# Kernel tuning notes

Hardware: AMD Instinct MI355X
Metric: run time of the kernel (lower is better)

Reference implementation:

```python
import jax, jax.numpy as jnp
import numpy as np

B, TAU, M, NX, NY = 256, 128, 3, 8, 8
N = NX + NY                 # 16 total sensors
D = 2 * N * N               # d_model = 512
NHEAD = 8
DFF = 2048


def _layer_norm(x, g, b, eps=1e-5):
    mu = jnp.mean(x, axis=-1, keepdims=True)
    var = jnp.mean((x - mu) ** 2, axis=-1, keepdims=True)
    return (x - mu) / jnp.sqrt(var + eps) * g + b


def _mha(x, wi, bi, wo, bo):
    Bq, S, Dm = x.shape
    hd = Dm // NHEAD
    qkv = x @ wi.T + bi                         # (B,S,3D)
    q, k, v = jnp.split(qkv, 3, axis=-1)
    sh = lambda t: t.reshape(Bq, S, NHEAD, hd).transpose(0, 2, 1, 3)
    q, k, v = sh(q), sh(k), sh(v)
    att = jax.nn.softmax(jnp.einsum('bhqd,bhkd->bhqk', q, k) / jnp.sqrt(jnp.float32(hd)), axis=-1)
    o = jnp.einsum('bhqk,bhkd->bhqd', att, v).transpose(0, 2, 1, 3).reshape(Bq, S, Dm)
    return o @ wo.T + bo


def poly_roots(c):
    # companion-matrix roots; c[..., 0] is the leading coefficient
    n = c.shape[-1] - 1
    first = (-c[..., 1:] / c[..., :1])[..., None, :]                      # (..., 1, n)
    below = jnp.broadcast_to(jnp.eye(n - 1, n, dtype=c.dtype), c.shape[:-1] + (n - 1, n))
    return jnp.linalg.eigvals(jnp.concatenate([first, below], axis=-2))   # (..., n)


def root_music_doa(Rz, m):
    # Rz: (B, n, n) Hermitian PSD (gram + eps*I) -> eigh == eig sorted by |lambda|
    n = Rz.shape[-1]
    w, v = jnp.linalg.eigh(Rz)                  # ascending real eigenvalues
    Un = v[..., : n - m]                        # noise subspace (smallest n-m)
    F = Un @ jnp.conj(jnp.swapaxes(Un, -1, -2))
    # sum of each diagonal, offsets -(n-1)..(n-1) -> 2n-1 poly coefficients
    coeffs = jnp.stack([jnp.sum(jnp.diagonal(F, offset=o, axis1=-2, axis2=-1), axis=-1)
                        for o in range(-(n - 1), n)], axis=-1)
    roots = poly_roots(coeffs)                  # (B, 2n-2)
    # sort by closeness to unit circle; push roots with |r|>=1 to the back
    keyv = jnp.abs(jnp.abs(roots) - 1.0) + jnp.where(jnp.abs(roots) < 1.0, 0.0, 1e6)
    sel = jnp.take_along_axis(roots, jnp.argsort(keyv, axis=-1)[..., :m], axis=-1)
    # dist=0.5, f=1 -> 1/(2*pi*dist*f) = 1/pi
    return jnp.arcsin(jnp.angle(sel) / jnp.pi)  # (B, m)


def setup_inputs() -> dict:
    key = jax.random.key(0)
    ks = jax.random.split(key, 12)
    rn = lambda k, s: 0.02 * jax.random.normal(k, s, jnp.float32)
    return {
        'Rx_tau': jax.random.normal(ks[0], (B, TAU, 2 * N, N), jnp.float32),
        'in_proj_w': rn(ks[1], (3 * D, D)), 'in_proj_b': jnp.zeros((3 * D,), jnp.float32),
        'out_proj_w': rn(ks[2], (D, D)), 'out_proj_b': jnp.zeros((D,), jnp.float32),
        'ln1_g': jnp.ones((D,), jnp.float32), 'ln1_b': jnp.zeros((D,), jnp.float32),
        'ffn_w1': rn(ks[3], (DFF, D)), 'ffn_b1': jnp.zeros((DFF,), jnp.float32),
        'ffn_w2': rn(ks[4], (D, DFF)), 'ffn_b2': jnp.zeros((D,), jnp.float32),
        'ln2_g': jnp.ones((D,), jnp.float32), 'ln2_b': jnp.zeros((D,), jnp.float32),
        'fcx_w': rn(ks[5], (2 * NX * NX, D)), 'fcx_b': jnp.zeros((2 * NX * NX,), jnp.float32),
        'fcy_w': rn(ks[6], (2 * NY * NY, D)), 'fcy_b': jnp.zeros((2 * NY * NY,), jnp.float32),
        'mlp_w1': rn(ks[7], (256, 2 * M)), 'mlp_b1': jnp.zeros((256,), jnp.float32),
        'mlp_w2': rn(ks[8], (256, 256)), 'mlp_b2': jnp.zeros((256,), jnp.float32),
        'mlp_w3': rn(ks[9], (2 * M, 256)), 'mlp_b3': jnp.zeros((2 * M,), jnp.float32),
    }


def reference(Rx_tau, in_proj_w, in_proj_b, out_proj_w, out_proj_b, ln1_g, ln1_b,
              ffn_w1, ffn_b1, ffn_w2, ffn_b2, ln2_g, ln2_b,
              fcx_w, fcx_b, fcy_w, fcy_b,
              mlp_w1, mlp_b1, mlp_w2, mlp_b2, mlp_w3, mlp_b3):
    x = Rx_tau.reshape(Rx_tau.shape[0], -1, D)  # (B, tau, 512)
    # post-LN TransformerEncoderLayer (eval: dropout off)
    x = _layer_norm(x + _mha(x, in_proj_w, in_proj_b, out_proj_w, out_proj_b), ln1_g, ln1_b)
    ff = jnp.maximum(x @ ffn_w1.T + ffn_b1, 0.0) @ ffn_w2.T + ffn_b2
    x = _layer_norm(x + ff, ln2_g, ln2_b)
    x = jnp.mean(x, axis=1)                     # (B, D)
    Rx = (x @ fcx_w.T + fcx_b).reshape(-1, 2 * NX, NX)
    Ry = (x @ fcy_w.T + fcy_b).reshape(-1, 2 * NY, NY)
    Kx = jax.lax.complex(Rx[:, :NX], Rx[:, NX:])
    Ky = jax.lax.complex(Ry[:, :NY], Ry[:, NY:])
    # gram_diagonal_overload: K^H K + eps*I, eps=1
    Rz_x = jnp.einsum('bji,bjk->bik', jnp.conj(Kx), Kx) + jnp.eye(NX, dtype=Kx.dtype)
    Rz_y = jnp.einsum('bji,bjk->bik', jnp.conj(Ky), Ky) + jnp.eye(NY, dtype=Ky.dtype)
    doa_t = root_music_doa(Rz_x, M)
    doa_p = root_music_doa(Rz_y, M)
    h = jnp.concatenate([doa_t, doa_p], axis=-1).astype(jnp.float32)  # (B, 2M)
    h = jnp.maximum(h @ mlp_w1.T + mlp_b1, 0.0)
    h = jnp.maximum(h @ mlp_w2.T + mlp_b2, 0.0)
    outs = h @ mlp_w3.T + mlp_b3
    return outs[:, :M], outs[:, M:]
```

## Files before the change

kernel.cpp:

```cpp
#include <hip/hip_runtime.h>
#include <math.h>

#define S_LEN 128
#define D_MODEL 512
#define B_SZ 256
#define NHEADS 8
#define HD 64
#define DFFN 2048
#define PI_D 3.14159265358979323846
#define DK_ITERS 128
#define JACOBI_SWEEPS 9

typedef _Float16 f16x8 __attribute__((ext_vector_type(8)));
typedef _Float16 f16x4 __attribute__((ext_vector_type(4)));
typedef float f32x4 __attribute__((ext_vector_type(4)));

__device__ __forceinline__ void gl_lds(const _Float16* g, _Float16* l) {
    __builtin_amdgcn_global_load_lds(
        (const __attribute__((address_space(1))) void*)g,
        (__attribute__((address_space(3))) void*)l, 16, 0, 0);
}

__global__ __launch_bounds__(256) void cvt_split(const float* __restrict__ in,
        _Float16* __restrict__ hi, _Float16* __restrict__ lo, int n4)
{
    const int i = blockIdx.x * 256 + threadIdx.x;
    if (i >= n4) return;
    float4 v = ((const float4*)in)[i];
    f16x4 h, l;
    _Float16 h0 = (_Float16)v.x; h[0] = h0; l[0] = (_Float16)(v.x - (float)h0);
    _Float16 h1 = (_Float16)v.y; h[1] = h1; l[1] = (_Float16)(v.y - (float)h1);
    _Float16 h2 = (_Float16)v.z; h[2] = h2; l[2] = (_Float16)(v.z - (float)h2);
    _Float16 h3 = (_Float16)v.w; h[3] = h3; l[3] = (_Float16)(v.w - (float)h3);
    ((f16x4*)hi)[i] = h;
    ((f16x4*)lo)[i] = l;
}

template<int OUTMODE>
__global__ __launch_bounds__(256) void gemm_mfma(
        const _Float16* __restrict__ Ahg, const _Float16* __restrict__ Alg,
        const _Float16* __restrict__ Whg, const _Float16* __restrict__ Wlg,
        const float* __restrict__ bias, float* __restrict__ Cf,
        _Float16* __restrict__ Ch, _Float16* __restrict__ Cl,
        int M, int N, int K)
{
    __shared__ _Float16 lds[2][4][4096];
    const int t = threadIdx.x;
    const int lane = t & 63;
    const int w = t >> 6;
    const int wr = w >> 1, wc = w & 1;
    const int row0 = blockIdx.y * 128, col0 = blockIdx.x * 128;

    const _Float16* gptr[4] = { Ahg, Alg, Whg, Wlg };
    const int rbase = (w < 2) ? row0 : col0;
    const _Float16* gsrc = gptr[w];
    const int lr = lane >> 2;
    const int lc = (lane & 3) * 8;

    auto stage = [&](int buf, int kt) {
        const _Float16* srcb = gsrc + (size_t)(rbase + lr) * K + (kt << 5) + lc;
        _Float16* dstb = &lds[buf][w][lane * 8];
#pragma unroll
        for (int p = 0; p < 8; ++p)
            gl_lds(srcb + (size_t)p * 16 * K, dstb + p * 512);
    };

    f32x4 acc[4][4];
#pragma unroll
    for (int m = 0; m < 4; ++m)
#pragma unroll
        for (int n = 0; n < 4; ++n) acc[m][n] = (f32x4)0.f;

    const int NT = K >> 5;
    stage(0, 0);
    float bv[4];
#pragma unroll
    for (int n = 0; n < 4; ++n) bv[n] = bias[col0 + wc * 64 + n * 16 + (lane & 15)];

    __syncthreads();

    const int kf = (lane >> 4) * 8;
    for (int kt = 0; kt < NT; ++kt) {
        const int cur = kt & 1;
        if (kt + 1 < NT) stage(cur ^ 1, kt + 1);
        f16x8 afh[4], afl[4], bfh[4], bfl[4];
#pragma unroll
        for (int m = 0; m < 4; ++m) {
            const int e = (wr * 64 + m * 16 + (lane & 15)) * 32 + kf;
            afh[m] = *(const f16x8*)&lds[cur][0][e];
            afl[m] = *(const f16x8*)&lds[cur][1][e];
        }
#pragma unroll
        for (int n = 0; n < 4; ++n) {
            const int e = (wc * 64 + n * 16 + (lane & 15)) * 32 + kf;
            bfh[n] = *(const f16x8*)&lds[cur][2][e];
            bfl[n] = *(const f16x8*)&lds[cur][3][e];
        }
#pragma unroll
        for (int m = 0; m < 4; ++m)
#pragma unroll
            for (int n = 0; n < 4; ++n) {
                acc[m][n] = __builtin_amdgcn_mfma_f32_16x16x32_f16(afh[m], bfh[n], acc[m][n], 0, 0, 0);
                acc[m][n] = __builtin_amdgcn_mfma_f32_16x16x32_f16(afh[m], bfl[n], acc[m][n], 0, 0, 0);
                acc[m][n] = __builtin_amdgcn_mfma_f32_16x16x32_f16(afl[m], bfh[n], acc[m][n], 0, 0, 0);
            }
        __syncthreads();
    }

#pragma unroll
    for (int m = 0; m < 4; ++m) {
        const int rowc = row0 + wr * 64 + m * 16 + ((lane >> 4) << 2);
#pragma unroll
        for (int n = 0; n < 4; ++n) {
            const int colc = col0 + wc * 64 + n * 16 + (lane & 15);
#pragma unroll
            for (int j = 0; j < 4; ++j) {
                float v = acc[m][n][j] + bv[n];
                if (OUTMODE == 2) {
                    v = fmaxf(v, 0.f);
                    const size_t idx = (size_t)(rowc + j) * N + colc;
                    _Float16 h = (_Float16)v;
                    Ch[idx] = h;
                    Cl[idx] = (_Float16)(v - (float)h);
                } else {
                    Cf[(size_t)(rowc + j) * N + colc] = v;
                }
            }
        }
    }
}

template<int RELU>
__global__ __launch_bounds__(256) void gemm_bias(const float* __restrict__ A,
        const float* __restrict__ W, const float* __restrict__ bias,
        float* __restrict__ C, int M, int N, int K)
{
    __shared__ float As[8][128];
    __shared__ float Ws[8][128];
    const int tid = threadIdx.x;
    const int tn = tid & 15, tm = tid >> 4;
    const int row0 = blockIdx.y * 128, col0 = blockIdx.x * 128;
    const int lrr = tid >> 1, lcc = (tid & 1) * 4;
    const float* Ap = A + (size_t)(row0 + lrr) * K + lcc;
    const float* Wp = W + (size_t)(col0 + lrr) * K + lcc;
    float acc[8][8];
#pragma unroll
    for (int i = 0; i < 8; ++i)
#pragma unroll
        for (int j = 0; j < 8; ++j) acc[i][j] = 0.f;

    for (int k0 = 0; k0 < K; k0 += 8) {
        float4 av = *(const float4*)(Ap + k0);
        float4 wv = *(const float4*)(Wp + k0);
        __syncthreads();
        As[lcc + 0][lrr] = av.x; As[lcc + 1][lrr] = av.y;
        As[lcc + 2][lrr] = av.z; As[lcc + 3][lrr] = av.w;
        Ws[lcc + 0][lrr] = wv.x; Ws[lcc + 1][lrr] = wv.y;
        Ws[lcc + 2][lrr] = wv.z; Ws[lcc + 3][lrr] = wv.w;
        __syncthreads();
#pragma unroll
        for (int k = 0; k < 8; ++k) {
            float ar[8], wrg[8];
#pragma unroll
            for (int i = 0; i < 8; ++i) ar[i] = As[k][tm * 8 + i];
#pragma unroll
            for (int j = 0; j < 8; ++j) wrg[j] = Ws[k][tn * 8 + j];
#pragma unroll
            for (int i = 0; i < 8; ++i)
#pragma unroll
                for (int j = 0; j < 8; ++j)
                    acc[i][j] = fmaf(ar[i], wrg[j], acc[i][j]);
        }
    }
#pragma unroll
    for (int i = 0; i < 8; ++i) {
        const int r = row0 + tm * 8 + i;
#pragma unroll
        for (int j = 0; j < 8; ++j) {
            const int c = col0 + tn * 8 + j;
            float v = acc[i][j] + bias[c];
            if (RELU) v = fmaxf(v, 0.f);
            C[(size_t)r * N + c] = v;
        }
    }
}

__global__ __launch_bounds__(128) void attn_kernel(const float* __restrict__ qkv,
        _Float16* __restrict__ oh, _Float16* __restrict__ ol)
{
    const int bh = blockIdx.x;
    const int b = bh >> 3, hh = bh & 7;
    const int t = threadIdx.x;
    __shared__ float Ks[S_LEN][HD];
    __shared__ float Vs[S_LEN][HD];
    const float* base = qkv + (size_t)b * S_LEN * (3 * D_MODEL);
    const float* krow = base + (size_t)t * (3 * D_MODEL) + D_MODEL + hh * HD;
    const float* vrow = base + (size_t)t * (3 * D_MODEL) + 2 * D_MODEL + hh * HD;
#pragma unroll
    for (int d = 0; d < HD; d += 4) {
        *(float4*)&Ks[t][d] = *(const float4*)(krow + d);
        *(float4*)&Vs[t][d] = *(const float4*)(vrow + d);
    }
    float q[HD];
    const float* qrow = base + (size_t)t * (3 * D_MODEL) + hh * HD;
#pragma unroll
    for (int d = 0; d < HD; d += 4) {
        float4 v4 = *(const float4*)(qrow + d);
        q[d] = v4.x; q[d + 1] = v4.y; q[d + 2] = v4.z; q[d + 3] = v4.w;
    }
    __syncthreads();
    float m = -1e30f, l = 0.f;
    float oacc[HD];
#pragma unroll
    for (int d = 0; d < HD; ++d) oacc[d] = 0.f;
    for (int j = 0; j < S_LEN; ++j) {
        float s = 0.f;
#pragma unroll
        for (int d = 0; d < HD; ++d) s = fmaf(q[d], Ks[j][d], s);
        s *= 0.125f;
        const float nm = fmaxf(m, s);
        const float sc = expf(m - nm);
        const float p = expf(s - nm);
        l = l * sc + p;
#pragma unroll
        for (int d = 0; d < HD; ++d) oacc[d] = oacc[d] * sc + p * Vs[j][d];
        m = nm;
    }
    const float inv = 1.f / l;
    const size_t ob = (size_t)b * S_LEN * D_MODEL + (size_t)t * D_MODEL + hh * HD;
#pragma unroll
    for (int d = 0; d < HD; ++d) {
        const float v = oacc[d] * inv;
        const _Float16 h = (_Float16)v;
        oh[ob + d] = h;
        ol[ob + d] = (_Float16)(v - (float)h);
    }
}

template<int SPLIT>
__global__ __launch_bounds__(128) void add_ln_kernel(const float* __restrict__ a,
        const float* __restrict__ bb, const float* __restrict__ g,
        const float* __restrict__ be, float* __restrict__ out,
        _Float16* __restrict__ oh, _Float16* __restrict__ ol)
{
    __shared__ float red[2];
    const int row = blockIdx.x, t = threadIdx.x;
    float4 av = *(const float4*)(a + (size_t)row * D_MODEL + t * 4);
    float4 bv = *(const float4*)(bb + (size_t)row * D_MODEL + t * 4);
    float x0 = av.x + bv.x, x1 = av.y + bv.y, x2 = av.z + bv.z, x3 = av.w + bv.w;
    float ssum = x0 + x1 + x2 + x3;
#pragma unroll
    for (int off = 32; off >= 1; off >>= 1) ssum += __shfl_xor(ssum, off);
    if ((t & 63) == 0) red[t >> 6] = ssum;
    __syncthreads();
    const float mean = (red[0] + red[1]) * (1.f / 512.f);
    __syncthreads();
    float d0 = x0 - mean, d1 = x1 - mean, d2 = x2 - mean, d3 = x3 - mean;
    float sq = d0 * d0 + d1 * d1 + d2 * d2 + d3 * d3;
#pragma unroll
    for (int off = 32; off >= 1; off >>= 1) sq += __shfl_xor(sq, off);
    if ((t & 63) == 0) red[t >> 6] = sq;
    __syncthreads();
    const float var = (red[0] + red[1]) * (1.f / 512.f);
    const float inv = 1.0f / sqrtf(var + 1e-5f);
    float4 gv = *(const float4*)(g + t * 4);
    float4 bev = *(const float4*)(be + t * 4);
    float4 ov = make_float4(d0 * inv * gv.x + bev.x, d1 * inv * gv.y + bev.y,
                            d2 * inv * gv.z + bev.z, d3 * inv * gv.w + bev.w);
    *(float4*)(out + (size_t)row * D_MODEL + t * 4) = ov;
    if (SPLIT) {
        f16x4 h, l;
        _Float16 h0 = (_Float16)ov.x; h[0] = h0; l[0] = (_Float16)(ov.x - (float)h0);
        _Float16 h1 = (_Float16)ov.y; h[1] = h1; l[1] = (_Float16)(ov.y - (float)h1);
        _Float16 h2 = (_Float16)ov.z; h[2] = h2; l[2] = (_Float16)(ov.z - (float)h2);
        _Float16 h3 = (_Float16)ov.w; h[3] = h3; l[3] = (_Float16)(ov.w - (float)h3);
        *(f16x4*)&oh[(size_t)row * D_MODEL + t * 4] = h;
        *(f16x4*)&ol[(size_t)row * D_MODEL + t * 4] = l;
    }
}

__global__ __launch_bounds__(128) void pool_kernel(const float* __restrict__ x,
                                                   float* __restrict__ pooled)
{
    const int b = blockIdx.x, t = threadIdx.x;
    float4 acc = make_float4(0.f, 0.f, 0.f, 0.f);
    const float* base = x + (size_t)b * S_LEN * D_MODEL + t * 4;
    for (int s = 0; s < S_LEN; ++s) {
        float4 v = *(const float4*)(base + (size_t)s * D_MODEL);
        acc.x += v.x; acc.y += v.y; acc.z += v.z; acc.w += v.w;
    }
    const float sc = 1.f / 128.f;
    float4 ov = make_float4(acc.x * sc, acc.y * sc, acc.z * sc, acc.w * sc);
    *(float4*)(pooled + (size_t)b * D_MODEL + t * 4) = ov;
}

__global__ __launch_bounds__(64) void music_kernel(const float* __restrict__ RxRy,
                                                   float* __restrict__ hbuf)
{
    const int pb = blockIdx.x;
    const int b = pb >> 1, which = pb & 1;
    const float* src = RxRy + (size_t)which * (B_SZ * 128) + (size_t)b * 128;
    const int t = threadIdx.x;
    const int i = t >> 3, j = t & 7;

    __shared__ double KRe[8][8], KIm[8][8];
    __shared__ double Ar[8][8], Ai[8][8], Vr[8][8], Vi[8][8];
    __shared__ double Fre[8][8], Fim[8][8];
    __shared__ double rc[4], rs[4], rer[4], rei[4];
    __shared__ double cr[15], ci[15], br[14], bi[14], zr[14], zi[14];
    __shared__ int topidx[3];

    KRe[i][j] = (double)src[i * 8 + j];
    KIm[i][j] = (double)src[64 + i * 8 + j];
    __syncthreads();
    {
        double sre = (i == j) ? 1.0 : 0.0, sim = 0.0;
        for (int r = 0; r < 8; ++r) {
            const double ar = KRe[r][i], ai = KIm[r][i];
            const double xr = KRe[r][j], xi = KIm[r][j];
            sre += ar * xr + ai * xi;
            sim += ar * xi - ai * xr;
        }
        Ar[i][j] = sre; Ai[i][j] = sim;
        Vr[i][j] = (i == j) ? 1.0 : 0.0;
        Vi[i][j] = 0.0;
    }
    __syncthreads();

    for (int sw = 0; sw < JACOBI_SWEEPS; ++sw)
    for (int rr = 0; rr < 7; ++rr) {
        int pp[4], qq[4];
        pp[0] = 0;                 qq[0] = (rr + 6) % 7 + 1;
        pp[1] = rr % 7 + 1;        qq[1] = (rr + 5) % 7 + 1;
        pp[2] = (rr + 1) % 7 + 1;  qq[2] = (rr + 4) % 7 + 1;
        pp[3] = (rr + 2) % 7 + 1;  qq[3] = (rr + 3) % 7 + 1;
        if (t < 4) {
            const int p = pp[t], q = qq[t];
            const double gre = Ar[p][q], gim = Ai[p][q];
            const double r = sqrt(gre * gre + gim * gim);
            double c, s, er, ei;
            if (r < 1e-60) { c = 1.0; s = 0.0; er = 1.0; ei = 0.0; }
            else {
                const double tau = (Ar[p][p] - Ar[q][q]) / (2.0 * r);
                const double tt = ((tau >= 0.0) ? 1.0 : -1.0) /
                                  (fabs(tau) + sqrt(1.0 + tau * tau));
                c = 1.0 / sqrt(1.0 + tt * tt); s = tt * c;
                er = gre / r; ei = gim / r;
            }
            rc[t] = c; rs[t] = s; rer[t] = er; rei[t] = ei;
        }
        __syncthreads();
        int gi = 0, gj = 0;
#pragma unroll
        for (int g = 0; g < 4; ++g) {
            if (pp[g] == i || qq[g] == i) gi = g;
            if (pp[g] == j || qq[g] == j) gj = g;
        }
        const int ri_q = (qq[gi] == i), rj_q = (qq[gj] == j);
        const double ci_ = rc[gi], si_ = rs[gi], eir = rer[gi], eii = rei[gi];
        const double cj_ = rc[gj], sj_ = rs[gj], ejr = rer[gj], eji = rei[gj];
        const int Pi = pp[gi], Qi = qq[gi], Pj = pp[gj], Qj = qq[gj];

        double bPr, bPi_, bQr, bQi_;
        {
            double apr = Ar[Pi][Pj], api = Ai[Pi][Pj];
            double aqr = Ar[Pi][Qj], aqi = Ai[Pi][Qj];
            if (!rj_q) { bPr = cj_ * apr + sj_ * (ejr * aqr + eji * aqi);
                         bPi_= cj_ * api + sj_ * (ejr * aqi - eji * aqr); }
            else       { bPr = cj_ * aqr - sj_ * (ejr * apr - eji * api);
                         bPi_= cj_ * aqi - sj_ * (ejr * api + eji * apr); }
            apr = Ar[Qi][Pj]; api = Ai[Qi][Pj];
            aqr = Ar[Qi][Qj]; aqi = Ai[Qi][Qj];
            if (!rj_q) { bQr = cj_ * apr + sj_ * (ejr * aqr + eji * aqi);
                         bQi_= cj_ * api + sj_ * (ejr * aqi - eji * aqr); }
            else       { bQr = cj_ * aqr - sj_ * (ejr * apr - eji * api);
                         bQi_= cj_ * aqi - sj_ * (ejr * api + eji * apr); }
        }
        double nAr, nAi_;
        if (!ri_q) { nAr = ci_ * bPr + si_ * (eir * bQr - eii * bQi_);
                     nAi_= ci_ * bPi_+ si_ * (eir * bQi_ + eii * bQr); }
        else       { nAr = ci_ * bQr - si_ * (eir * bPr + eii * bPi_);
                     nAi_= ci_ * bQi_- si_ * (eir * bPi_ - eii * bPr); }
        double nVr, nVi_;
        {
            const double vpr = Vr[i][Pj], vpi = Vi[i][Pj];
            const double vqr = Vr[i][Qj], vqi = Vi[i][Qj];
            if (!rj_q) { nVr = cj_ * vpr + sj_ * (ejr * vqr + eji * vqi);
                         nVi_= cj_ * vpi + sj_ * (ejr * vqi - eji * vqr); }
            else       { nVr = cj_ * vqr - sj_ * (ejr * vpr - eji * vpi);
                         nVi_= cj_ * vqi - sj_ * (ejr * vpi + eji * vpr); }
        }
        __syncthreads();
        Ar[i][j] = nAr; Ai[i][j] = nAi_;
        Vr[i][j] = nVr; Vi[i][j] = nVi_;
        __syncthreads();
    }

    if (t == 0) {
        bool used[8] = {false, false, false, false, false, false, false, false};
        for (int tt = 0; tt < 3; ++tt) {
            double best = -1e300; int bidx = 0;
            for (int k = 0; k < 8; ++k)
                if (!used[k] && Ar[k][k] > best) { best = Ar[k][k]; bidx = k; }
            used[bidx] = true; topidx[tt] = bidx;
        }
    }
    __syncthreads();
    {
        double fre = (i == j) ? 1.0 : 0.0, fim = 0.0;
        for (int tt = 0; tt < 3; ++tt) {
            const int e = topidx[tt];
            const double vir = Vr[i][e], vii = Vi[i][e];
            const double vjr = Vr[j][e], vji = Vi[j][e];
            fre -= vir * vjr + vii * vji;
            fim -= vii * vjr - vir * vji;
        }
        Fre[i][j] = fre; Fim[i][j] = fim;
    }
    __syncthreads();
    if (t < 15) {
        const int o = t - 7;
        double sre = 0.0, sim = 0.0;
        for (int r = 0; r < 8; ++r) {
            const int cc = r + o;
            if (cc >= 0 && cc < 8) { sre += Fre[r][cc]; sim += Fim[r][cc]; }
        }
        cr[t] = sre; ci[t] = sim;
    }
    __syncthreads();
    if (t < 14) {
        const double den = cr[0] * cr[0] + ci[0] * ci[0];
        const double nr = cr[t + 1], ni = ci[t + 1];
        br[t] = (nr * cr[0] + ni * ci[0]) / den;
        bi[t] = (ni * cr[0] - nr * ci[0]) / den;
        double zre_ = 1.0, zim_ = 0.0;
        for (int k = 0; k <= t; ++k) {
            const double a2 = zre_ * 0.4 - zim_ * 0.9;
            zim_ = zre_ * 0.9 + zim_ * 0.4;
            zre_ = a2;
        }
        zr[t] = zre_; zi[t] = zim_;
    }
    __syncthreads();

    const int rt = t >> 2, jj = t & 3;
    const int rsafe = (rt < 14) ? rt : 0;
    double A_r[4], A_i[4];
#pragma unroll
    for (int m = 0; m < 4; ++m) {
        const int idx = 13 - 4 * m - jj;
        if (idx >= 0)       { A_r[m] = br[idx]; A_i[m] = bi[idx]; }
        else if (idx == -1) { A_r[m] = 1.0;     A_i[m] = 0.0; }
        else                { A_r[m] = 0.0;     A_i[m] = 0.0; }
    }
    const int k0 = jj * 4, k1 = (jj == 3) ? 14 : jj * 4 + 4;

    for (int it = 0; it < DK_ITERS; ++it) {
        const double zre = zr[rsafe], zim = zi[rsafe];
        const double z2r = zre * zre - zim * zim, z2i = 2.0 * zre * zim;
        const double yr = z2r * z2r - z2i * z2i, yi = 2.0 * z2r * z2i;
        double wre = A_r[3], wim = A_i[3];
#pragma unroll
        for (int m = 2; m >= 0; --m) {
            const double tr = wre * yr - wim * yi + A_r[m];
            wim = wre * yi + wim * yr + A_i[m];
            wre = tr;
        }
        double pr, pi;
        if (jj == 0)      { pr = wre; pi = wim; }
        else if (jj == 1) { pr = wre * zre - wim * zim; pi = wre * zim + wim * zre; }
        else if (jj == 2) { pr = wre * z2r - wim * z2i; pi = wre * z2i + wim * z2r; }
        else { const double z3r = z2r * zre - z2i * zim, z3i = z2r * zim + z2i * zre;
               pr = wre * z3r - wim * z3i; pi = wre * z3i + wim * z3r; }
        pr += __shfl_xor(pr, 1); pi += __shfl_xor(pi, 1);
        pr += __shfl_xor(pr, 2); pi += __shfl_xor(pi, 2);
        double dr = 1.0, di = 0.0;
        for (int k = k0; k < k1; ++k) {
            if (k == rsafe) continue;
            const double exr = zre - zr[k], exi = zim - zi[k];
            const double tr = dr * exr - di * exi;
            di = dr * exi + di * exr;
            dr = tr;
        }
        {
            double orr = __shfl_xor(dr, 1), oii = __shfl_xor(di, 1);
            double tr = dr * orr - di * oii; di = dr * oii + di * orr; dr = tr;
            orr = __shfl_xor(dr, 2); oii = __shfl_xor(di, 2);
            tr = dr * orr - di * oii; di = dr * oii + di * orr; dr = tr;
        }
        double nzr, nzi;
        const double dd = dr * dr + di * di;
        if (dd > 1e-260) {
            const double qre = (pr * dr + pi * di) / dd;
            const double qim = (pi * dr - pr * di) / dd;
            nzr = zre - qre; nzi = zim - qim;
        } else {
            nzr = zre + 1e-8; nzi = zim - 1e-8;
        }
        __syncthreads();
        if (t < 56 && jj == 0) { zr[rt] = nzr; zi[rt] = nzi; }
        __syncthreads();
    }

    if (t == 0) {
        double keyv[14]; bool used[14];
        for (int k = 0; k < 14; ++k) {
            const double mag = sqrt(zr[k] * zr[k] + zi[k] * zi[k]);
            keyv[k] = fabs(mag - 1.0) + ((mag < 1.0) ? 0.0 : 1e6);
            used[k] = false;
        }
        for (int tt = 0; tt < 3; ++tt) {
            double best = 1e300; int bidx = 0;
            for (int k = 0; k < 14; ++k)
                if (!used[k] && keyv[k] < best) { best = keyv[k]; bidx = k; }
            used[bidx] = true;
            const double ang = atan2(zi[bidx], zr[bidx]);
            double ratio = ang / PI_D;
            if (ratio > 1.0) ratio = 1.0;
            if (ratio < -1.0) ratio = -1.0;
            hbuf[(size_t)b * 6 + which * 3 + tt] = (float)asin(ratio);
        }
    }
}

__global__ __launch_bounds__(256) void mlp_kernel(const float* __restrict__ hbuf,
        const float* __restrict__ w1, const float* __restrict__ b1,
        const float* __restrict__ w2, const float* __restrict__ b2,
        const float* __restrict__ w3, const float* __restrict__ b3,
        float* __restrict__ outp)
{
    const int b = blockIdx.x, t = threadIdx.x;
    __shared__ float hin[8];
    __shared__ float h1[256];
    __shared__ float h2[256];
    if (t < 6) hin[t] = hbuf[b * 6 + t];
    __syncthreads();
    float acc = b1[t];
#pragma unroll
    for (int k = 0; k < 6; ++k) acc += hin[k] * w1[t * 6 + k];
    h1[t] = fmaxf(acc, 0.f);
    __syncthreads();
    float acc2 = b2[t];
    for (int k = 0; k < 256; ++k) acc2 += h1[k] * w2[t * 256 + k];
    h2[t] = fmaxf(acc2, 0.f);
    __syncthreads();
    if (t < 6) {
        float acc3 = b3[t];
        for (int k = 0; k < 256; ++k) acc3 += h2[k] * w3[t * 256 + k];
        if (t < 3) outp[b * 3 + t] = acc3;
        else       outp[B_SZ * 3 + b * 3 + (t - 3)] = acc3;
    }
}

extern "C" void kernel_launch(void* const* d_in, const int* in_sizes, int n_in,
                              void* d_out, int out_size, void* d_ws, size_t ws_size,
                              hipStream_t stream)
{
    const float* x_in      = (const float*)d_in[0];
    const float* in_proj_w = (const float*)d_in[1];
    const float* in_proj_b = (const float*)d_in[2];
    const float* out_proj_w= (const float*)d_in[3];
    const float* out_proj_b= (const float*)d_in[4];
    const float* ln1_g     = (const float*)d_in[5];
    const float* ln1_b     = (const float*)d_in[6];
    const float* ffn_w1    = (const float*)d_in[7];
    const float* ffn_b1    = (const float*)d_in[8];
    const float* ffn_w2    = (const float*)d_in[9];
    const float* ffn_b2    = (const float*)d_in[10];
    const float* ln2_g     = (const float*)d_in[11];
    const float* ln2_b     = (const float*)d_in[12];
    const float* fcx_w     = (const float*)d_in[13];
    const float* fcx_b     = (const float*)d_in[14];
    const float* fcy_w     = (const float*)d_in[15];
    const float* fcy_b     = (const float*)d_in[16];
    const float* mlp_w1    = (const float*)d_in[17];
    const float* mlp_b1    = (const float*)d_in[18];
    const float* mlp_w2    = (const float*)d_in[19];
    const float* mlp_b2    = (const float*)d_in[20];
    const float* mlp_w3    = (const float*)d_in[21];
    const float* mlp_b3    = (const float*)d_in[22];

    const size_t N_IPW = 1536 * 512, N_OPW = 512 * 512;
    const size_t N_F1W = 2048 * 512, N_F2W = 512 * 2048;
    const size_t WCVT = N_IPW + N_OPW + N_F1W + N_F2W;
    float* ws = (float*)d_ws;
    _Float16* ipw_h = (_Float16*)ws;
    _Float16* ipw_l = ipw_h + N_IPW;
    _Float16* opw_h = ipw_l + N_IPW;
    _Float16* opw_l = opw_h + N_OPW;
    _Float16* f1w_h = opw_l + N_OPW;
    _Float16* f1w_l = f1w_h + N_F1W;
    _Float16* f2w_h = f1w_l + N_F1W;
    _Float16* f2w_l = f2w_h + N_F2W;
    float* dyn = ws + WCVT;

    const size_t ws_floats = ws_size / sizeof(float);
    int c = 256;
    while (c > 1 && (size_t)524288 * (size_t)c + 262144 + WCVT > ws_floats) c >>= 1;

    float* R0     = dyn;
    float* xhf    = R0 + (size_t)262144 * c;
    float* xlf    = xhf + (size_t)32768 * c;
    float* x1     = xlf + (size_t)32768 * c;
    float* x1hf   = x1 + (size_t)65536 * c;
    float* x1lf   = x1hf + (size_t)32768 * c;
    float* ff2    = x1lf + (size_t)32768 * c;
    float* pooled = ff2 + (size_t)65536 * c;
    float* RxRy   = pooled + 131072;
    float* hbuf   = RxRy + 65536;

    float*    qkv  = R0;
    _Float16* oh   = (_Float16*)(R0 + (size_t)196608 * c);
    _Float16* ol   = oh + (size_t)65536 * c;
    _Float16* ff1h = (_Float16*)R0;
    _Float16* ff1l = ff1h + (size_t)262144 * c;
    _Float16* xh   = (_Float16*)xhf;
    _Float16* xl   = (_Float16*)xlf;
    _Float16* x1h  = (_Float16*)x1hf;
    _Float16* x1l  = (_Float16*)x1lf;

    cvt_split<<<(N_IPW / 4 + 255) / 256, 256, 0, stream>>>(in_proj_w,  ipw_h, ipw_l, N_IPW / 4);
    cvt_split<<<(N_OPW / 4 + 255) / 256, 256, 0, stream>>>(out_proj_w, opw_h, opw_l, N_OPW / 4);
    cvt_split<<<(N_F1W / 4 + 255) / 256, 256, 0, stream>>>(ffn_w1,     f1w_h, f1w_l, N_F1W / 4);
    cvt_split<<<(N_F2W / 4 + 255) / 256, 256, 0, stream>>>(ffn_w2,     f2w_h, f2w_l, N_F2W / 4);

    for (int b0 = 0; b0 < B_SZ; b0 += c) {
        const int Tc = c * S_LEN;
        const float* xc = x_in + (size_t)b0 * S_LEN * D_MODEL;
        const int n4x = Tc * D_MODEL / 4;

        cvt_split<<<(n4x + 255) / 256, 256, 0, stream>>>(xc, xh, xl, n4x);
        gemm_mfma<0><<<dim3(1536 / 128, Tc / 128), 256, 0, stream>>>(
            xh, xl, ipw_h, ipw_l, in_proj_b, qkv, nullptr, nullptr, Tc, 3 * D_MODEL, D_MODEL);
        attn_kernel<<<c * NHEADS, 128, 0, stream>>>(qkv, oh, ol);
        gemm_mfma<0><<<dim3(512 / 128, Tc / 128), 256, 0, stream>>>(
            oh, ol, opw_h, opw_l, out_proj_b, x1, nullptr, nullptr, Tc, D_MODEL, D_MODEL);
        add_ln_kernel<1><<<Tc, 128, 0, stream>>>(xc, x1, ln1_g, ln1_b, x1, x1h, x1l);
        gemm_mfma<2><<<dim3(DFFN / 128, Tc / 128), 256, 0, stream>>>(
            x1h, x1l, f1w_h, f1w_l, ffn_b1, nullptr, ff1h, ff1l, Tc, DFFN, D_MODEL);
        gemm_mfma<0><<<dim3(512 / 128, Tc / 128), 256, 0, stream>>>(
            ff1h, ff1l, f2w_h, f2w_l, ffn_b2, ff2, nullptr, nullptr, Tc, D_MODEL, DFFN);
        add_ln_kernel<0><<<Tc, 128, 0, stream>>>(x1, ff2, ln2_g, ln2_b, x1, nullptr, nullptr);
        pool_kernel<<<c, 128, 0, stream>>>(x1, pooled + (size_t)b0 * D_MODEL);
    }

    gemm_bias<0><<<dim3(1, 2), 256, 0, stream>>>(
        pooled, fcx_w, fcx_b, RxRy, B_SZ, 128, D_MODEL);
    gemm_bias<0><<<dim3(1, 2), 256, 0, stream>>>(
        pooled, fcy_w, fcy_b, RxRy + B_SZ * 128, B_SZ, 128, D_MODEL);
    music_kernel<<<2 * B_SZ, 64, 0, stream>>>(RxRy, hbuf);
    mlp_kernel<<<B_SZ, 256, 0, stream>>>(hbuf, mlp_w1, mlp_b1, mlp_w2, mlp_b2,
                                         mlp_w3, mlp_b3, (float*)d_out);
}
```

Baseline: 1.661 ms.

## Load GEMM fragments directly to registers; keep Durand-Kerner roots in registers via shuffles

The split-fp16 MFMA GEMM no longer stages tiles through LDS with global_load_lds and barriers. Each wave now loads its fragments straight from global memory into two register sets, ping-ponged so loads overlap MFMA work, with launch bounds asking for 2 blocks per CU. This removes LDS traffic and __syncthreads, but drops the data reuse that LDS gave across waves, so global/L2 reads rise and register pressure grows. Separately, the Durand-Kerner root iteration keeps each root in registers and reads the other roots with wave shuffles, removing the two block barriers per iteration.

```diff
diff --git a/kernel.cpp b/kernel.cpp
--- a/kernel.cpp
+++ b/kernel.cpp
@@ -14,12 +14,6 @@
 typedef _Float16 f16x8 __attribute__((ext_vector_type(8)));
 typedef _Float16 f16x4 __attribute__((ext_vector_type(4)));
 typedef float f32x4 __attribute__((ext_vector_type(4)));
-
-__device__ __forceinline__ void gl_lds(const _Float16* g, _Float16* l) {
-    __builtin_amdgcn_global_load_lds(
-        (const __attribute__((address_space(1))) void*)g,
-        (__attribute__((address_space(3))) void*)l, 16, 0, 0);
-}
 
 __global__ __launch_bounds__(256) void cvt_split(const float* __restrict__ in,
         _Float16* __restrict__ hi, _Float16* __restrict__ lo, int n4)
@@ -36,34 +30,48 @@
     ((f16x4*)lo)[i] = l;
 }
 
+
+#define LOADSET(AH, AL, BH, BL, KT) do {                                      \
+    const size_t kk_ = (size_t)(KT) * 32;                                     \
+    _Pragma("unroll")                                                         \
+    for (int m_ = 0; m_ < 4; ++m_) {                                          \
+        AH[m_] = *(const f16x8*)(Ahg + aoff + (size_t)m_ * 16 * K + kk_);     \
+        AL[m_] = *(const f16x8*)(Alg + aoff + (size_t)m_ * 16 * K + kk_);     \
+        BH[m_] = *(const f16x8*)(Whg + boff + (size_t)m_ * 16 * K + kk_);     \
+        BL[m_] = *(const f16x8*)(Wlg + boff + (size_t)m_ * 16 * K + kk_);     \
+    }                                                                         \
+} while (0)
+
+#define COMPUTE(AH, AL, BH, BL) do {                                          \
+    _Pragma("unroll")                                                         \
+    for (int m_ = 0; m_ < 4; ++m_)                                            \
+    _Pragma("unroll")                                                         \
+    for (int n_ = 0; n_ < 4; ++n_) {                                          \
+        acc[m_][n_] = __builtin_amdgcn_mfma_f32_16x16x32_f16(AH[m_], BH[n_], acc[m_][n_], 0, 0, 0); \
+        acc[m_][n_] = __builtin_amdgcn_mfma_f32_16x16x32_f16(AH[m_], BL[n_], acc[m_][n_], 0, 0, 0); \
+        acc[m_][n_] = __builtin_amdgcn_mfma_f32_16x16x32_f16(AL[m_], BH[n_], acc[m_][n_], 0, 0, 0); \
+    }                                                                         \
+} while (0)
+
 template<int OUTMODE>
-__global__ __launch_bounds__(256) void gemm_mfma(
+__global__ __launch_bounds__(256, 2) void gemm_mfma(
         const _Float16* __restrict__ Ahg, const _Float16* __restrict__ Alg,
         const _Float16* __restrict__ Whg, const _Float16* __restrict__ Wlg,
         const float* __restrict__ bias, float* __restrict__ Cf,
         _Float16* __restrict__ Ch, _Float16* __restrict__ Cl,
         int M, int N, int K)
 {
-    __shared__ _Float16 lds[2][4][4096];
     const int t = threadIdx.x;
     const int lane = t & 63;
     const int w = t >> 6;
     const int wr = w >> 1, wc = w & 1;
     const int row0 = blockIdx.y * 128, col0 = blockIdx.x * 128;
 
-    const _Float16* gptr[4] = { Ahg, Alg, Whg, Wlg };
-    const int rbase = (w < 2) ? row0 : col0;
-    const _Float16* gsrc = gptr[w];
-    const int lr = lane >> 2;
-    const int lc = (lane & 3) * 8;
-
-    auto stage = [&](int buf, int kt) {
-        const _Float16* srcb = gsrc + (size_t)(rbase + lr) * K + (kt << 5) + lc;
-        _Float16* dstb = &lds[buf][w][lane * 8];
-#pragma unroll
-        for (int p = 0; p < 8; ++p)
-            gl_lds(srcb + (size_t)p * 16 * K, dstb + p * 512);
-    };
+    const int fr = lane & 15;
+    const int kg = (lane >> 4) * 8;
+
+    const size_t aoff = (size_t)(row0 + wr * 64 + fr) * K + kg;
+    const size_t boff = (size_t)(col0 + wc * 64 + fr) * K + kg;
 
     f32x4 acc[4][4];
 #pragma unroll
@@ -71,40 +79,20 @@
 #pragma unroll
         for (int n = 0; n < 4; ++n) acc[m][n] = (f32x4)0.f;
 
+    float bv[4];
+#pragma unroll
+    for (int n = 0; n < 4; ++n) bv[n] = bias[col0 + wc * 64 + n * 16 + fr];
+
+    f16x8 ah0[4], al0[4], bh0[4], bl0[4];
+    f16x8 ah1[4], al1[4], bh1[4], bl1[4];
+
     const int NT = K >> 5;
-    stage(0, 0);
-    float bv[4];
-#pragma unroll
-    for (int n = 0; n < 4; ++n) bv[n] = bias[col0 + wc * 64 + n * 16 + (lane & 15)];
-
-    __syncthreads();
-
-    const int kf = (lane >> 4) * 8;
-    for (int kt = 0; kt < NT; ++kt) {
-        const int cur = kt & 1;
-        if (kt + 1 < NT) stage(cur ^ 1, kt + 1);
-        f16x8 afh[4], afl[4], bfh[4], bfl[4];
-#pragma unroll
-        for (int m = 0; m < 4; ++m) {
-            const int e = (wr * 64 + m * 16 + (lane & 15)) * 32 + kf;
-            afh[m] = *(const f16x8*)&lds[cur][0][e];
-            afl[m] = *(const f16x8*)&lds[cur][1][e];
-        }
-#pragma unroll
-        for (int n = 0; n < 4; ++n) {
-            const int e = (wc * 64 + n * 16 + (lane & 15)) * 32 + kf;
-            bfh[n] = *(const f16x8*)&lds[cur][2][e];
-            bfl[n] = *(const f16x8*)&lds[cur][3][e];
-        }
-#pragma unroll
-        for (int m = 0; m < 4; ++m)
-#pragma unroll
-            for (int n = 0; n < 4; ++n) {
-                acc[m][n] = __builtin_amdgcn_mfma_f32_16x16x32_f16(afh[m], bfh[n], acc[m][n], 0, 0, 0);
-                acc[m][n] = __builtin_amdgcn_mfma_f32_16x16x32_f16(afh[m], bfl[n], acc[m][n], 0, 0, 0);
-                acc[m][n] = __builtin_amdgcn_mfma_f32_16x16x32_f16(afl[m], bfh[n], acc[m][n], 0, 0, 0);
-            }
-        __syncthreads();
+    LOADSET(ah0, al0, bh0, bl0, 0);
+    for (int kt = 0; kt < NT; kt += 2) {
+        if (kt + 1 < NT) LOADSET(ah1, al1, bh1, bl1, kt + 1);
+        COMPUTE(ah0, al0, bh0, bl0);
+        if (kt + 2 < NT) LOADSET(ah0, al0, bh0, bl0, kt + 2);
+        if (kt + 1 < NT) COMPUTE(ah1, al1, bh1, bl1);
     }
 
 #pragma unroll
@@ -112,7 +100,7 @@
         const int rowc = row0 + wr * 64 + m * 16 + ((lane >> 4) << 2);
 #pragma unroll
         for (int n = 0; n < 4; ++n) {
-            const int colc = col0 + wc * 64 + n * 16 + (lane & 15);
+            const int colc = col0 + wc * 64 + n * 16 + fr;
 #pragma unroll
             for (int j = 0; j < 4; ++j) {
                 float v = acc[m][n][j] + bv[n];
@@ -433,13 +421,6 @@
         const double nr = cr[t + 1], ni = ci[t + 1];
         br[t] = (nr * cr[0] + ni * ci[0]) / den;
         bi[t] = (ni * cr[0] - nr * ci[0]) / den;
-        double zre_ = 1.0, zim_ = 0.0;
-        for (int k = 0; k <= t; ++k) {
-            const double a2 = zre_ * 0.4 - zim_ * 0.9;
-            zim_ = zre_ * 0.9 + zim_ * 0.4;
-            zre_ = a2;
-        }
-        zr[t] = zre_; zi[t] = zim_;
     }
     __syncthreads();
 
@@ -453,10 +434,19 @@
         else if (idx == -1) { A_r[m] = 1.0;     A_i[m] = 0.0; }
         else                { A_r[m] = 0.0;     A_i[m] = 0.0; }
     }
-    const int k0 = jj * 4, k1 = (jj == 3) ? 14 : jj * 4 + 4;
+
+    double zre, zim;
+    {
+        double zr_ = 1.0, zi_ = 0.0;
+        for (int k = 0; k <= rsafe; ++k) {
+            const double a2 = zr_ * 0.4 - zi_ * 0.9;
+            zi_ = zr_ * 0.9 + zi_ * 0.4;
+            zr_ = a2;
+        }
+        zre = zr_; zim = zi_;
+    }
 
     for (int it = 0; it < DK_ITERS; ++it) {
-        const double zre = zr[rsafe], zim = zi[rsafe];
         const double z2r = zre * zre - zim * zim, z2i = 2.0 * zre * zim;
         const double yr = z2r * z2r - z2i * z2i, yi = 2.0 * z2r * z2i;
         double wre = A_r[3], wim = A_i[3];
@@ -475,12 +465,17 @@
         pr += __shfl_xor(pr, 1); pi += __shfl_xor(pi, 1);
         pr += __shfl_xor(pr, 2); pi += __shfl_xor(pi, 2);
         double dr = 1.0, di = 0.0;
-        for (int k = k0; k < k1; ++k) {
-            if (k == rsafe) continue;
-            const double exr = zre - zr[k], exi = zim - zi[k];
-            const double tr = dr * exr - di * exi;
+#pragma unroll
+        for (int q = 0; q < 4; ++q) {
+            const int k = jj * 4 + q;
+            const double zkr = __shfl(zre, 4 * k);
+            const double zki = __shfl(zim, 4 * k);
+            const bool val = (k < 14) && (k != rsafe);
+            const double exr = val ? (zre - zkr) : 1.0;
+            const double exi = val ? (zim - zki) : 0.0;
+            const double trd = dr * exr - di * exi;
             di = dr * exi + di * exr;
-            dr = tr;
+            dr = trd;
         }
         {
             double orr = __shfl_xor(dr, 1), oii = __shfl_xor(di, 1);
@@ -488,19 +483,17 @@
             orr = __shfl_xor(dr, 2); oii = __shfl_xor(di, 2);
             tr = dr * orr - di * oii; di = dr * oii + di * orr; dr = tr;
         }
-        double nzr, nzi;
         const double dd = dr * dr + di * di;
         if (dd > 1e-260) {
             const double qre = (pr * dr + pi * di) / dd;
             const double qim = (pi * dr - pr * di) / dd;
-            nzr = zre - qre; nzi = zim - qim;
+            zre = zre - qre; zim = zim - qim;
         } else {
-            nzr = zre + 1e-8; nzi = zim - 1e-8;
-        }
-        __syncthreads();
-        if (t < 56 && jj == 0) { zr[rt] = nzr; zi[rt] = nzi; }
-        __syncthreads();
-    }
+            zre = zre + 1e-8; zim = zim - 1e-8;
+        }
+    }
+    if (rt < 14 && jj == 0) { zr[rt] = zre; zi[rt] = zim; }
+    __syncthreads();
 
     if (t == 0) {
         double keyv[14]; bool used[14];
```

Measured after the change: 2.400 ms. 44.5% more time.
